# Performance work log

Measured on AMD Instinct MI355X. Metric: run time of the kernel, lower is better.

Reference implementation:

```python
import jax, jax.numpy as jnp
import numpy as np

N_NODES = 100000
N_EDGES = 1600000
NFEAT = 256
NHID = 128


def setup_inputs() -> dict:
    key = jax.random.key(0)
    ks = jax.random.split(key, 8)
    x = jax.random.normal(ks[0], (N_NODES, NFEAT), dtype=jnp.float32)
    edge_row = jax.random.randint(ks[1], (N_EDGES,), 0, N_NODES, dtype=jnp.int32)
    edge_col = jax.random.randint(ks[2], (N_EDGES,), 0, N_NODES, dtype=jnp.int32)
    edge_val = jax.random.uniform(ks[3], (N_EDGES,), dtype=jnp.float32)
    # Glorot-ish init for the two GraphConvolution weights
    W1 = jax.random.normal(ks[4], (NFEAT, NHID), dtype=jnp.float32) * (1.0 / np.sqrt(NFEAT))
    b1 = jnp.zeros((NHID,), dtype=jnp.float32)
    W2 = jax.random.normal(ks[5], (NHID, NHID), dtype=jnp.float32) * (1.0 / np.sqrt(NHID))
    b2 = jnp.zeros((NHID,), dtype=jnp.float32)
    return {"x": x, "edge_row": edge_row, "edge_col": edge_col,
            "edge_val": edge_val, "W1": W1, "b1": b1, "W2": W2, "b2": b2}


def _gcn_layer(h, W, b, edge_row, edge_col, edge_val, n_nodes):
    # support = h @ W  (dense transform), then spmm(adj, support) + b
    support = h @ W                              # [N, d_out]
    msgs = edge_val[:, None] * support[edge_col]  # [E, d_out] gather
    agg = jax.ops.segment_sum(msgs, edge_row, num_segments=n_nodes)  # scatter-add
    return agg + b


def reference(x, edge_row, edge_col, edge_val, W1, b1, W2, b2):
    n = x.shape[0]
    # eval mode: dropout is identity
    h = jax.nn.relu(_gcn_layer(x, W1, b1, edge_row, edge_col, edge_val, n))
    for _ in range(4):  # gc2 applied 4 times with shared weights
        h = jax.nn.relu(_gcn_layer(h, W2, b2, edge_row, edge_col, edge_val, n))
    return h
```

## Files before the change

kernel.cpp:

```cpp
#include <hip/hip_runtime.h>

constexpr int NFEAT = 256;
constexpr int NHID  = 128;
constexpr int SCAN_B = 4096;


__global__ void hist_kernel(const int* __restrict__ rows, int* __restrict__ cnt, int n) {
  int i = blockIdx.x * blockDim.x + threadIdx.x;
  if (i < n) atomicAdd(&cnt[rows[i]], 1);
}

__global__ void scan1_kernel(const int* __restrict__ cnt, int* __restrict__ part,
                             int* __restrict__ bsum, int n) {
  __shared__ int tmp[1024];
  int tid = threadIdx.x;
  int base = blockIdx.x * SCAN_B + tid * 4;
  int4 v = make_int4(0, 0, 0, 0);
  if (base + 4 <= n) {
    v = *(const int4*)&cnt[base];
  } else {
    if (base + 0 < n) v.x = cnt[base + 0];
    if (base + 1 < n) v.y = cnt[base + 1];
    if (base + 2 < n) v.z = cnt[base + 2];
    if (base + 3 < n) v.w = cnt[base + 3];
  }
  int s = v.x + v.y + v.z + v.w;
  tmp[tid] = s;
  __syncthreads();
  for (int off = 1; off < 1024; off <<= 1) {
    int t = (tid >= off) ? tmp[tid - off] : 0;
    __syncthreads();
    tmp[tid] += t;
    __syncthreads();
  }
  int excl = tmp[tid] - s;
  if (base + 0 < n) part[base + 0] = excl;
  if (base + 1 < n) part[base + 1] = excl + v.x;
  if (base + 2 < n) part[base + 2] = excl + v.x + v.y;
  if (base + 3 < n) part[base + 3] = excl + v.x + v.y + v.z;
  if (tid == 1023) bsum[blockIdx.x] = tmp[1023];
}

__global__ void scan2_kernel(int* __restrict__ bsum, int nb) {
  if (threadIdx.x == 0 && blockIdx.x == 0) {
    int run = 0;
    for (int i = 0; i < nb; ++i) { int t = bsum[i]; bsum[i] = run; run += t; }
    bsum[nb] = run;
  }
}

__global__ void scan3_kernel(int* __restrict__ row_ptr, const int* __restrict__ bsum,
                             int* __restrict__ cursor, int n, int nb) {
  int i = blockIdx.x * blockDim.x + threadIdx.x;
  if (i < n) {
    int v = row_ptr[i] + bsum[i / SCAN_B];
    row_ptr[i] = v;
    cursor[i]  = v;
  }
  if (i == 0) row_ptr[n] = bsum[nb];
}

__global__ void scatter_kernel(const int* __restrict__ rows, const int* __restrict__ cols,
                               const float* __restrict__ vals, int* __restrict__ cursor,
                               int* __restrict__ cols_s, float* __restrict__ vals_s, int n) {
  int i = blockIdx.x * blockDim.x + threadIdx.x;
  if (i < n) {
    int p = atomicAdd(&cursor[rows[i]], 1);
    cols_s[p] = cols[i];
    vals_s[p] = vals[i];
  }
}


__global__ __launch_bounds__(256) void gemm_kernel(const float* __restrict__ A,
                                                   const float* __restrict__ W,
                                                   float* __restrict__ C, int M, int K) {
  __shared__ float As[32][132];
  __shared__ float Bs[32][128];
  int tid = threadIdx.x;
  int block_row = blockIdx.x * 128;
  int r8 = tid >> 4;
  int c8 = tid & 15;
  float acc[2][2][4][4] = {};

  for (int k0 = 0; k0 < K; k0 += 32) {
    #pragma unroll
    for (int i = 0; i < 4; ++i) {
      int f = tid + i * 256;
      int row = f >> 3;
      int kq = (f & 7) * 4;
      int grow = block_row + row;
      float4 av = make_float4(0.f, 0.f, 0.f, 0.f);
      if (grow < M) av = *(const float4*)&A[(size_t)grow * K + k0 + kq];
      As[kq + 0][row] = av.x; As[kq + 1][row] = av.y;
      As[kq + 2][row] = av.z; As[kq + 3][row] = av.w;
    }
    #pragma unroll
    for (int i = 0; i < 4; ++i) {
      int f = tid + i * 256;
      int r = f >> 5;
      int cq = (f & 31) * 4;
      *(float4*)&Bs[r][cq] = *(const float4*)&W[(size_t)(k0 + r) * 128 + cq];
    }
    __syncthreads();
    #pragma unroll
    for (int kk = 0; kk < 32; ++kk) {
      float4 a0 = *(const float4*)&As[kk][r8 * 4];
      float4 a1 = *(const float4*)&As[kk][r8 * 4 + 64];
      float4 b0 = *(const float4*)&Bs[kk][c8 * 4];
      float4 b1 = *(const float4*)&Bs[kk][c8 * 4 + 64];
      float ar[2][4] = {{a0.x, a0.y, a0.z, a0.w}, {a1.x, a1.y, a1.z, a1.w}};
      float br[2][4] = {{b0.x, b0.y, b0.z, b0.w}, {b1.x, b1.y, b1.z, b1.w}};
      #pragma unroll
      for (int rh = 0; rh < 2; ++rh)
        #pragma unroll
        for (int i = 0; i < 4; ++i)
          #pragma unroll
          for (int ch = 0; ch < 2; ++ch)
            #pragma unroll
            for (int j = 0; j < 4; ++j)
              acc[rh][ch][i][j] += ar[rh][i] * br[ch][j];
    }
    __syncthreads();
  }

  #pragma unroll
  for (int rh = 0; rh < 2; ++rh)
    #pragma unroll
    for (int i = 0; i < 4; ++i) {
      int grow = block_row + rh * 64 + r8 * 4 + i;
      if (grow < M) {
        #pragma unroll
        for (int ch = 0; ch < 2; ++ch) {
          float4 v = make_float4(acc[rh][ch][i][0], acc[rh][ch][i][1],
                                 acc[rh][ch][i][2], acc[rh][ch][i][3]);
          *(float4*)&C[(size_t)grow * 128 + ch * 64 + c8 * 4] = v;
        }
      }
    }
}


__global__ void spmm_kernel(const float* __restrict__ support, const int* __restrict__ row_ptr,
                            const int* __restrict__ cols, const float* __restrict__ vals,
                            const float* __restrict__ bias, float* __restrict__ out, int n_nodes) {
  int row  = blockIdx.x * (blockDim.x >> 6) + (threadIdx.x >> 6);
  int lane = threadIdx.x & 63;
  if (row >= n_nodes) return;
  int beg = row_ptr[row], end = row_ptr[row + 1];
  float accx = 0.f, accy = 0.f;
  for (int chunk = beg; chunk < end; chunk += 64) {
    int idx = chunk + lane;
    int m = min(64, end - chunk);
    int cl = (idx < end) ? cols[idx] : 0;
    float vl = (idx < end) ? vals[idx] : 0.f;
    int e = 0;
    for (; e + 4 <= m; e += 4) {
      int c0 = __shfl(cl, e),     c1 = __shfl(cl, e + 1);
      int c2 = __shfl(cl, e + 2), c3 = __shfl(cl, e + 3);
      float v0 = __shfl(vl, e),     v1 = __shfl(vl, e + 1);
      float v2 = __shfl(vl, e + 2), v3 = __shfl(vl, e + 3);
      float2 s0 = *(const float2*)&support[(size_t)c0 * 128 + lane * 2];
      float2 s1 = *(const float2*)&support[(size_t)c1 * 128 + lane * 2];
      float2 s2 = *(const float2*)&support[(size_t)c2 * 128 + lane * 2];
      float2 s3 = *(const float2*)&support[(size_t)c3 * 128 + lane * 2];
      accx += v0 * s0.x; accy += v0 * s0.y;
      accx += v1 * s1.x; accy += v1 * s1.y;
      accx += v2 * s2.x; accy += v2 * s2.y;
      accx += v3 * s3.x; accy += v3 * s3.y;
    }
    for (; e < m; ++e) {
      int ce = __shfl(cl, e);
      float ve = __shfl(vl, e);
      float2 s = *(const float2*)&support[(size_t)ce * 128 + lane * 2];
      accx += ve * s.x; accy += ve * s.y;
    }
  }
  float2 b = *(const float2*)&bias[lane * 2];
  float2 o = make_float2(fmaxf(accx + b.x, 0.f), fmaxf(accy + b.y, 0.f));
  *(float2*)&out[(size_t)row * 128 + lane * 2] = o;
}


extern "C" void kernel_launch(void* const* d_in, const int* in_sizes, int n_in,
                              void* d_out, int out_size, void* d_ws, size_t ws_size,
                              hipStream_t stream) {
  const float* x    = (const float*)d_in[0];
  const int*   erow = (const int*)d_in[1];
  const int*   ecol = (const int*)d_in[2];
  const float* evl  = (const float*)d_in[3];
  const float* W1   = (const float*)d_in[4];
  const float* b1   = (const float*)d_in[5];
  const float* W2   = (const float*)d_in[6];
  const float* b2   = (const float*)d_in[7];
  int n_nodes = in_sizes[0] / NFEAT;
  int n_edges = in_sizes[1];
  float* out = (float*)d_out;

  char* ws = (char*)d_ws;
  size_t off = 0;
  auto alloc = [&](size_t bytes) -> void* {
    void* p = ws + off;
    off += bytes;
    off = (off + 255) & ~(size_t)255;
    return p;
  };
  float* support = (float*)alloc((size_t)n_nodes * NHID * sizeof(float));
  int*   cnt     = (int*)alloc((size_t)n_nodes * sizeof(int));
  int*   row_ptr = (int*)alloc(((size_t)n_nodes + 1) * sizeof(int));
  int*   cursor  = (int*)alloc((size_t)n_nodes * sizeof(int));
  int*   cols_s  = (int*)alloc((size_t)n_edges * sizeof(int));
  float* vals_s  = (float*)alloc((size_t)n_edges * sizeof(float));
  int nb = (n_nodes + SCAN_B - 1) / SCAN_B;
  int*   bsum    = (int*)alloc((size_t)(nb + 1) * sizeof(int));

  hipMemsetAsync(cnt, 0, (size_t)n_nodes * sizeof(int), stream);
  hist_kernel<<<(n_edges + 255) / 256, 256, 0, stream>>>(erow, cnt, n_edges);
  scan1_kernel<<<nb, 1024, 0, stream>>>(cnt, row_ptr, bsum, n_nodes);
  scan2_kernel<<<1, 64, 0, stream>>>(bsum, nb);
  scan3_kernel<<<(n_nodes + 255) / 256, 256, 0, stream>>>(row_ptr, bsum, cursor, n_nodes, nb);
  scatter_kernel<<<(n_edges + 255) / 256, 256, 0, stream>>>(erow, ecol, evl, cursor,
                                                            cols_s, vals_s, n_edges);

  int gblocks = (n_nodes + 127) / 128;
  int sblocks = (n_nodes + 3) / 4;

  gemm_kernel<<<gblocks, 256, 0, stream>>>(x, W1, support, n_nodes, NFEAT);
  spmm_kernel<<<sblocks, 256, 0, stream>>>(support, row_ptr, cols_s, vals_s, b1, out, n_nodes);

  for (int l = 0; l < 4; ++l) {
    gemm_kernel<<<gblocks, 256, 0, stream>>>(out, W2, support, n_nodes, NHID);
    spmm_kernel<<<sblocks, 256, 0, stream>>>(support, row_ptr, cols_s, vals_s, b2, out, n_nodes);
  }
}
```

Before: 1.078 ms.

## Pack CSR edges, prefetch GEMM tiles with swizzled smem, unroll SpMM deeper

Column indices and values are now packed into one int2 array, so SpMM reads each edge with a single load. The GEMM is templated on K, moves to 64-row tiles with 128 threads, and prefetches the next k-tile into registers while computing the current one. It also stores A transposed into shared memory with an XOR swizzle to avoid bank conflicts. The SpMM inner loop unrolls to 8 gathers with two accumulator pairs to raise memory-level parallelism, at the cost of more registers and a slightly different summation order.

```diff
diff --git a/kernel.cpp b/kernel.cpp
--- a/kernel.cpp
+++ b/kernel.cpp
@@ -62,53 +62,83 @@
 
 __global__ void scatter_kernel(const int* __restrict__ rows, const int* __restrict__ cols,
                                const float* __restrict__ vals, int* __restrict__ cursor,
-                               int* __restrict__ cols_s, float* __restrict__ vals_s, int n) {
+                               int2* __restrict__ ev_s, int n) {
   int i = blockIdx.x * blockDim.x + threadIdx.x;
   if (i < n) {
     int p = atomicAdd(&cursor[rows[i]], 1);
-    cols_s[p] = cols[i];
-    vals_s[p] = vals[i];
-  }
-}
-
-
-__global__ __launch_bounds__(256) void gemm_kernel(const float* __restrict__ A,
+    ev_s[p] = make_int2(cols[i], __float_as_int(vals[i]));
+  }
+}
+
+
+template<int K>
+__global__ __launch_bounds__(128) void gemm_kernel(const float* __restrict__ A,
                                                    const float* __restrict__ W,
-                                                   float* __restrict__ C, int M, int K) {
-  __shared__ float As[32][132];
-  __shared__ float Bs[32][128];
+                                                   float* __restrict__ C, int M) {
+  __shared__ float As[32 * 64];
+  __shared__ float Bs[32 * 128];
   int tid = threadIdx.x;
-  int block_row = blockIdx.x * 128;
+  int block_row = blockIdx.x * 64;
   int r8 = tid >> 4;
   int c8 = tid & 15;
+  int rq  = tid >> 3;
+  int kq8 = tid & 7;
+
   float acc[2][2][4][4] = {};
-
-  for (int k0 = 0; k0 < K; k0 += 32) {
-    #pragma unroll
-    for (int i = 0; i < 4; ++i) {
-      int f = tid + i * 256;
-      int row = f >> 3;
-      int kq = (f & 7) * 4;
-      int grow = block_row + row;
-      float4 av = make_float4(0.f, 0.f, 0.f, 0.f);
-      if (grow < M) av = *(const float4*)&A[(size_t)grow * K + k0 + kq];
-      As[kq + 0][row] = av.x; As[kq + 1][row] = av.y;
-      As[kq + 2][row] = av.z; As[kq + 3][row] = av.w;
-    }
-    #pragma unroll
-    for (int i = 0; i < 4; ++i) {
-      int f = tid + i * 256;
-      int r = f >> 5;
-      int cq = (f & 31) * 4;
-      *(float4*)&Bs[r][cq] = *(const float4*)&W[(size_t)(k0 + r) * 128 + cq];
-    }
-    __syncthreads();
+  float4 t0, t1, t2, t3;
+  float4 bv[8];
+
+  auto loadA = [&](int k0) {
+    int gr = block_row + rq * 4;
+    const float* a0p = A + (size_t)(gr + 0) * K + k0 + kq8 * 4;
+    const float* a1p = A + (size_t)(gr + 1) * K + k0 + kq8 * 4;
+    const float* a2p = A + (size_t)(gr + 2) * K + k0 + kq8 * 4;
+    const float* a3p = A + (size_t)(gr + 3) * K + k0 + kq8 * 4;
+    float4 z = make_float4(0.f, 0.f, 0.f, 0.f);
+    t0 = (gr + 0 < M) ? *(const float4*)a0p : z;
+    t1 = (gr + 1 < M) ? *(const float4*)a1p : z;
+    t2 = (gr + 2 < M) ? *(const float4*)a2p : z;
+    t3 = (gr + 3 < M) ? *(const float4*)a3p : z;
+  };
+  auto loadB = [&](int k0) {
+    #pragma unroll
+    for (int i = 0; i < 8; ++i) {
+      int f = tid + i * 128;
+      bv[i] = *(const float4*)&W[(size_t)(k0 + (f >> 5)) * 128 + (f & 31) * 4];
+    }
+  };
+  auto storeAB = [&]() {
+    float4 w0 = make_float4(t0.x, t1.x, t2.x, t3.x);
+    float4 w1 = make_float4(t0.y, t1.y, t2.y, t3.y);
+    float4 w2 = make_float4(t0.z, t1.z, t2.z, t3.z);
+    float4 w3 = make_float4(t0.w, t1.w, t2.w, t3.w);
+    #pragma unroll
+    for (int j = 0; j < 4; ++j) {
+      int k = kq8 * 4 + j;
+      int idx = (k * 64 + rq * 4) ^ ((k & 7) << 2);
+      float4 w = (j == 0) ? w0 : (j == 1) ? w1 : (j == 2) ? w2 : w3;
+      *(float4*)&As[idx] = w;
+    }
+    #pragma unroll
+    for (int i = 0; i < 8; ++i) {
+      int f = tid + i * 128;
+      *(float4*)&Bs[(f >> 5) * 128 + (f & 31) * 4] = bv[i];
+    }
+  };
+
+  constexpr int NT = K / 32;
+  loadA(0); loadB(0);
+  for (int t = 0; t < NT; ++t) {
+    __syncthreads();
+    storeAB();
+    __syncthreads();
+    if (t + 1 < NT) { loadA((t + 1) * 32); loadB((t + 1) * 32); }
     #pragma unroll
     for (int kk = 0; kk < 32; ++kk) {
-      float4 a0 = *(const float4*)&As[kk][r8 * 4];
-      float4 a1 = *(const float4*)&As[kk][r8 * 4 + 64];
-      float4 b0 = *(const float4*)&Bs[kk][c8 * 4];
-      float4 b1 = *(const float4*)&Bs[kk][c8 * 4 + 64];
+      float4 a0 = *(const float4*)&As[(kk * 64 + r8 * 4) ^ ((kk & 7) << 2)];
+      float4 a1 = *(const float4*)&As[(kk * 64 + 32 + r8 * 4) ^ ((kk & 7) << 2)];
+      float4 b0 = *(const float4*)&Bs[kk * 128 + c8 * 4];
+      float4 b1 = *(const float4*)&Bs[kk * 128 + 64 + c8 * 4];
       float ar[2][4] = {{a0.x, a0.y, a0.z, a0.w}, {a1.x, a1.y, a1.z, a1.w}};
       float br[2][4] = {{b0.x, b0.y, b0.z, b0.w}, {b1.x, b1.y, b1.z, b1.w}};
       #pragma unroll
@@ -121,14 +151,13 @@
             for (int j = 0; j < 4; ++j)
               acc[rh][ch][i][j] += ar[rh][i] * br[ch][j];
     }
-    __syncthreads();
   }
 
   #pragma unroll
   for (int rh = 0; rh < 2; ++rh)
     #pragma unroll
     for (int i = 0; i < 4; ++i) {
-      int grow = block_row + rh * 64 + r8 * 4 + i;
+      int grow = block_row + rh * 32 + r8 * 4 + i;
       if (grow < M) {
         #pragma unroll
         for (int ch = 0; ch < 2; ++ch) {
@@ -142,40 +171,54 @@
 
 
 __global__ void spmm_kernel(const float* __restrict__ support, const int* __restrict__ row_ptr,
-                            const int* __restrict__ cols, const float* __restrict__ vals,
-                            const float* __restrict__ bias, float* __restrict__ out, int n_nodes) {
+                            const int2* __restrict__ ev, const float* __restrict__ bias,
+                            float* __restrict__ out, int n_nodes) {
   int row  = blockIdx.x * (blockDim.x >> 6) + (threadIdx.x >> 6);
   int lane = threadIdx.x & 63;
   if (row >= n_nodes) return;
   int beg = row_ptr[row], end = row_ptr[row + 1];
-  float accx = 0.f, accy = 0.f;
+  float ax0 = 0.f, ay0 = 0.f, ax1 = 0.f, ay1 = 0.f;
   for (int chunk = beg; chunk < end; chunk += 64) {
     int idx = chunk + lane;
     int m = min(64, end - chunk);
-    int cl = (idx < end) ? cols[idx] : 0;
-    float vl = (idx < end) ? vals[idx] : 0.f;
+    int2 ee = (idx < end) ? ev[idx] : make_int2(0, 0);
+    int cl = ee.x;
+    float vl = __int_as_float(ee.y);
     int e = 0;
-    for (; e + 4 <= m; e += 4) {
-      int c0 = __shfl(cl, e),     c1 = __shfl(cl, e + 1);
-      int c2 = __shfl(cl, e + 2), c3 = __shfl(cl, e + 3);
-      float v0 = __shfl(vl, e),     v1 = __shfl(vl, e + 1);
+    for (; e + 8 <= m; e += 8) {
+      int   c0 = __shfl(cl, e + 0), c1 = __shfl(cl, e + 1);
+      int   c2 = __shfl(cl, e + 2), c3 = __shfl(cl, e + 3);
+      int   c4 = __shfl(cl, e + 4), c5 = __shfl(cl, e + 5);
+      int   c6 = __shfl(cl, e + 6), c7 = __shfl(cl, e + 7);
+      float v0 = __shfl(vl, e + 0), v1 = __shfl(vl, e + 1);
       float v2 = __shfl(vl, e + 2), v3 = __shfl(vl, e + 3);
+      float v4 = __shfl(vl, e + 4), v5 = __shfl(vl, e + 5);
+      float v6 = __shfl(vl, e + 6), v7 = __shfl(vl, e + 7);
       float2 s0 = *(const float2*)&support[(size_t)c0 * 128 + lane * 2];
       float2 s1 = *(const float2*)&support[(size_t)c1 * 128 + lane * 2];
       float2 s2 = *(const float2*)&support[(size_t)c2 * 128 + lane * 2];
       float2 s3 = *(const float2*)&support[(size_t)c3 * 128 + lane * 2];
-      accx += v0 * s0.x; accy += v0 * s0.y;
-      accx += v1 * s1.x; accy += v1 * s1.y;
-      accx += v2 * s2.x; accy += v2 * s2.y;
-      accx += v3 * s3.x; accy += v3 * s3.y;
+      float2 s4 = *(const float2*)&support[(size_t)c4 * 128 + lane * 2];
+      float2 s5 = *(const float2*)&support[(size_t)c5 * 128 + lane * 2];
+      float2 s6 = *(const float2*)&support[(size_t)c6 * 128 + lane * 2];
+      float2 s7 = *(const float2*)&support[(size_t)c7 * 128 + lane * 2];
+      ax0 += v0 * s0.x; ay0 += v0 * s0.y;
+      ax1 += v1 * s1.x; ay1 += v1 * s1.y;
+      ax0 += v2 * s2.x; ay0 += v2 * s2.y;
+      ax1 += v3 * s3.x; ay1 += v3 * s3.y;
+      ax0 += v4 * s4.x; ay0 += v4 * s4.y;
+      ax1 += v5 * s5.x; ay1 += v5 * s5.y;
+      ax0 += v6 * s6.x; ay0 += v6 * s6.y;
+      ax1 += v7 * s7.x; ay1 += v7 * s7.y;
     }
     for (; e < m; ++e) {
-      int ce = __shfl(cl, e);
+      int   ce = __shfl(cl, e);
       float ve = __shfl(vl, e);
       float2 s = *(const float2*)&support[(size_t)ce * 128 + lane * 2];
-      accx += ve * s.x; accy += ve * s.y;
-    }
-  }
+      ax0 += ve * s.x; ay0 += ve * s.y;
+    }
+  }
+  float accx = ax0 + ax1, accy = ay0 + ay1;
   float2 b = *(const float2*)&bias[lane * 2];
   float2 o = make_float2(fmaxf(accx + b.x, 0.f), fmaxf(accy + b.y, 0.f));
   *(float2*)&out[(size_t)row * 128 + lane * 2] = o;
@@ -209,8 +252,7 @@
   int*   cnt     = (int*)alloc((size_t)n_nodes * sizeof(int));
   int*   row_ptr = (int*)alloc(((size_t)n_nodes + 1) * sizeof(int));
   int*   cursor  = (int*)alloc((size_t)n_nodes * sizeof(int));
-  int*   cols_s  = (int*)alloc((size_t)n_edges * sizeof(int));
-  float* vals_s  = (float*)alloc((size_t)n_edges * sizeof(float));
+  int2*  ev_s    = (int2*)alloc((size_t)n_edges * sizeof(int2));
   int nb = (n_nodes + SCAN_B - 1) / SCAN_B;
   int*   bsum    = (int*)alloc((size_t)(nb + 1) * sizeof(int));
 
@@ -220,16 +262,16 @@
   scan2_kernel<<<1, 64, 0, stream>>>(bsum, nb);
   scan3_kernel<<<(n_nodes + 255) / 256, 256, 0, stream>>>(row_ptr, bsum, cursor, n_nodes, nb);
   scatter_kernel<<<(n_edges + 255) / 256, 256, 0, stream>>>(erow, ecol, evl, cursor,
-                                                            cols_s, vals_s, n_edges);
-
-  int gblocks = (n_nodes + 127) / 128;
+                                                            ev_s, n_edges);
+
+  int gblocks = (n_nodes + 63) / 64;
   int sblocks = (n_nodes + 3) / 4;
 
-  gemm_kernel<<<gblocks, 256, 0, stream>>>(x, W1, support, n_nodes, NFEAT);
-  spmm_kernel<<<sblocks, 256, 0, stream>>>(support, row_ptr, cols_s, vals_s, b1, out, n_nodes);
+  gemm_kernel<NFEAT><<<gblocks, 128, 0, stream>>>(x, W1, support, n_nodes);
+  spmm_kernel<<<sblocks, 256, 0, stream>>>(support, row_ptr, ev_s, b1, out, n_nodes);
 
   for (int l = 0; l < 4; ++l) {
-    gemm_kernel<<<gblocks, 256, 0, stream>>>(out, W2, support, n_nodes, NHID);
-    spmm_kernel<<<sblocks, 256, 0, stream>>>(support, row_ptr, cols_s, vals_s, b2, out, n_nodes);
-  }
-}
+    gemm_kernel<NHID><<<gblocks, 128, 0, stream>>>(out, W2, support, n_nodes);
+    spmm_kernel<<<sblocks, 256, 0, stream>>>(support, row_ptr, ev_s, b2, out, n_nodes);
+  }
+}
```

Result: slower. 1.253 ms (+16.2%).
